# Kernel tuning notes

Hardware: AMD Instinct MI355X
Metric: run time of the kernel (lower is better)

The kernel has to match this reference:

```python
import jax, jax.numpy as jnp
import numpy as np

N_NODES = 50000
N_EDGES = 800000
N_GRAPHS = 512
NODE_IN = 128
EDGE_IN = 64
HIDDEN = 128
SHARED = 64


def setup_inputs() -> dict:
    key = jax.random.key(0)
    ks = jax.random.split(key, 24)
    def lin(k, fan_in, fan_out):
        lim = 1.0 / np.sqrt(fan_in)
        kw, kb = jax.random.split(k)
        w = jax.random.uniform(kw, (fan_in, fan_out), jnp.float32, -lim, lim)
        b = jax.random.uniform(kb, (fan_out,), jnp.float32, -lim, lim)
        return w, b
    x = jax.random.normal(ks[0], (N_NODES, NODE_IN), jnp.float32)
    edge_index = jax.random.randint(ks[1], (2, N_EDGES), 0, N_NODES, jnp.int64)
    edge_attr = jax.random.normal(ks[2], (N_EDGES, EDGE_IN), jnp.float32)
    batch = jnp.sort(jax.random.randint(ks[3], (N_NODES,), 0, N_GRAPHS, jnp.int64))
    e1_w, e1_b = lin(ks[4], EDGE_IN, NODE_IN)
    n1_w1, n1_b1 = lin(ks[5], NODE_IN, HIDDEN)
    n1_w2, n1_b2 = lin(ks[6], HIDDEN, HIDDEN)
    e2_w, e2_b = lin(ks[7], EDGE_IN, HIDDEN)
    n2_w1, n2_b1 = lin(ks[8], HIDDEN, HIDDEN)
    n2_w2, n2_b2 = lin(ks[9], HIDDEN, HIDDEN)
    fc_w, fc_b = lin(ks[10], HIDDEN, SHARED)
    hS_w, hS_b = lin(ks[11], SHARED, 1)
    hP_w, hP_b = lin(ks[12], SHARED, 1)
    hN_w, hN_b = lin(ks[13], SHARED, 1)
    return dict(x=x, edge_index=edge_index, edge_attr=edge_attr, batch=batch,
                e1_w=e1_w, e1_b=e1_b, n1_w1=n1_w1, n1_b1=n1_b1, n1_w2=n1_w2, n1_b2=n1_b2,
                e2_w=e2_w, e2_b=e2_b, n2_w1=n2_w1, n2_b1=n2_b1, n2_w2=n2_w2, n2_b2=n2_b2,
                fc_w=fc_w, fc_b=fc_b, hS_w=hS_w, hS_b=hS_b, hP_w=hP_w, hP_b=hP_b,
                hN_w=hN_w, hN_b=hN_b)


def gine_conv(x, edge_index, edge_attr, ew, eb, w1, b1, w2, b2):
    # message: relu(x_j + Lin(edge_attr)); aggregate: scatter-sum to target;
    # update: MLP((1 + eps) * x_i + aggr) with eps = 0 (PyG default)
    e = edge_attr @ ew + eb                      # [E, C]
    m = jax.nn.relu(x[edge_index[0]] + e)        # gather + fused add/relu
    aggr = jax.ops.segment_sum(m, edge_index[1], num_segments=N_NODES)
    h = x + aggr
    return jax.nn.relu(h @ w1 + b1) @ w2 + b2


def global_mean_pool(x, batch):
    sums = jax.ops.segment_sum(x, batch, num_segments=N_GRAPHS)
    cnt = jax.ops.segment_sum(jnp.ones((x.shape[0],), x.dtype), batch, num_segments=N_GRAPHS)
    return sums / jnp.maximum(cnt, 1.0)[:, None]


def reference(x, edge_index, edge_attr, batch,
              e1_w, e1_b, n1_w1, n1_b1, n1_w2, n1_b2,
              e2_w, e2_b, n2_w1, n2_b1, n2_w2, n2_b2,
              fc_w, fc_b, hS_w, hS_b, hP_w, hP_b, hN_w, hN_b):
    h = jax.nn.relu(gine_conv(x, edge_index, edge_attr, e1_w, e1_b, n1_w1, n1_b1, n1_w2, n1_b2))
    h = jax.nn.relu(gine_conv(h, edge_index, edge_attr, e2_w, e2_b, n2_w1, n2_b1, n2_w2, n2_b2))
    g = global_mean_pool(h, batch)               # [G, HIDDEN]
    s = jax.nn.relu(g @ fc_w + fc_b)             # [G, SHARED]
    logS = (s @ hS_w + hS_b)[:, 0]
    logP = (s @ hP_w + hP_b)[:, 0]
    nr = (s @ hN_w + hN_b)[:, 0]
    return logS, logP, nr
```

## Files before the change

### kernel.cpp

```cpp
#include <hip/hip_runtime.h>
#include <hip/hip_bf16.h>


typedef __bf16 bf16_t;

#define N_NODES   50000
#define N_EDGES   800000
#define N_GRAPHS  512
#define HID       128
#define EIN       64
#define PNODES    16

#define RL(v, l)  __int_as_float(__builtin_amdgcn_readlane(__float_as_int(v), (l)))
#define RLI(v, l) __builtin_amdgcn_readlane((v), (l))

__device__ __forceinline__ float ldf(const void* p, size_t i, int f32m) {
    return f32m ? ((const float*)p)[i] : (float)((const bf16_t*)p)[i];
}
__device__ __forceinline__ int ldi(const void* p, size_t i, int i64m) {
    return i64m ? (int)((const long long*)p)[i] : ((const int*)p)[i];
}

__global__ void k_detect(const unsigned short* __restrict__ xw,
                         const unsigned int*   __restrict__ eiw,
                         int* __restrict__ flags)
{
    if (threadIdx.x == 0 && blockIdx.x == 0) {
        int sane = 0;
        for (int i = 0; i < 256; ++i) {
            int e = (xw[i] >> 7) & 0xFF;
            if (e >= 100 && e <= 150) ++sane;
        }
        flags[0] = (sane < 220) ? 1 : 0;
        int nzhigh = 0;
        for (int i = 0; i < 256; ++i)
            if (eiw[2*i + 1] != 0) ++nzhigh;
        flags[1] = (nzhigh == 0) ? 1 : 0;
    }
}

__global__ void k_cvt4(const void* __restrict__ x, float* __restrict__ dst,
                       const int* __restrict__ flags) {
    const int f32m = flags[0];
    size_t i = (size_t)blockIdx.x * 256 + threadIdx.x;
    if (f32m) {
        ((float4*)dst)[i] = ((const float4*)x)[i];
    } else {
        const bf16_t* s = (const bf16_t*)x;
        float4 v;
        v.x = (float)s[4*i+0]; v.y = (float)s[4*i+1];
        v.z = (float)s[4*i+2]; v.w = (float)s[4*i+3];
        ((float4*)dst)[i] = v;
    }
}

__global__ __launch_bounds__(512) void k_edge_s(
        const void* __restrict__ Xg, int xg_ws,
        const void* __restrict__ ei,
        const void* __restrict__ ea,
        const void* __restrict__ ew,
        const void* __restrict__ eb,
        float*      __restrict__ ag,
        const int*  __restrict__ flags)
{
    __shared__ float4 Wq[16 * 128];
    __shared__ float  ebs[HID];
    const int f32m = flags[0];
    const int i64m = flags[1];
    const int xgf  = xg_ws ? 1 : f32m;

    for (int i = threadIdx.x; i < 16 * 128; i += 512) {
        int k4 = i >> 7, c = i & 127;
        float4 w;
        w.x = ldf(ew, (size_t)(4*k4+0)*HID + c, f32m);
        w.y = ldf(ew, (size_t)(4*k4+1)*HID + c, f32m);
        w.z = ldf(ew, (size_t)(4*k4+2)*HID + c, f32m);
        w.w = ldf(ew, (size_t)(4*k4+3)*HID + c, f32m);
        Wq[i] = w;
    }
    for (int i = threadIdx.x; i < HID; i += 512) ebs[i] = ldf(eb, i, f32m);
    __syncthreads();

    const int lane = threadIdx.x & 63;
    const int wid  = (blockIdx.x * 512 + threadIdx.x) >> 6;
    const int nw   = gridDim.x * 8;
    const int ngrp = N_EDGES / 8;
    const float eb0 = ebs[lane], eb1 = ebs[64 + lane];

    auto LOADIDX = [&](int e0) -> int {
        int v = 0;
        if (lane < 16) {
            size_t idx = (lane < 8) ? (size_t)(e0 + lane)
                                    : (size_t)N_EDGES + (e0 + lane - 8);
            v = ldi(ei, idx, i64m);
        }
        return v;
    };

    int g = wid;
    if (g < ngrp) {
        float avA[8]; int vvA;
        {
            const int e0 = g * 8;
            vvA = LOADIDX(e0);
#pragma unroll
            for (int i = 0; i < 8; ++i)
                avA[i] = ldf(ea, (size_t)(e0+i) * EIN + lane, f32m);
        }

        while (true) {
            const int gB = g + nw;
            const bool hasB = (gB < ngrp);
            float avB[8]; int vvB = 0;
            if (hasB) {
                const int e0B = gB * 8;
                vvB = LOADIDX(e0B);
#pragma unroll
                for (int i = 0; i < 8; ++i)
                    avB[i] = ldf(ea, (size_t)(e0B+i) * EIN + lane, f32m);
            }

            int src[8], dst[8];
#pragma unroll
            for (int i = 0; i < 8; ++i) {
                src[i] = RLI(vvA, i);
                dst[i] = RLI(vvA, 8 + i);
            }
            float x0[8], x1[8];
#pragma unroll
            for (int i = 0; i < 8; ++i) {
                x0[i] = ldf(Xg, (size_t)src[i] * HID + lane,      xgf);
                x1[i] = ldf(Xg, (size_t)src[i] * HID + 64 + lane, xgf);
            }

            float acc0[8], acc1[8];
#pragma unroll
            for (int i = 0; i < 8; ++i) { acc0[i] = 0.f; acc1[i] = 0.f; }

#pragma unroll 4
            for (int k4 = 0; k4 < 16; ++k4) {
                float4 w0 = Wq[k4 * 128 + lane];
                float4 w1 = Wq[k4 * 128 + 64 + lane];
#pragma unroll
                for (int i = 0; i < 8; ++i) {
                    float a0 = RL(avA[i], 4*k4+0);
                    float a1 = RL(avA[i], 4*k4+1);
                    float a2 = RL(avA[i], 4*k4+2);
                    float a3 = RL(avA[i], 4*k4+3);
                    acc0[i] = fmaf(a3, w0.w, fmaf(a2, w0.z, fmaf(a1, w0.y, fmaf(a0, w0.x, acc0[i]))));
                    acc1[i] = fmaf(a3, w1.w, fmaf(a2, w1.z, fmaf(a1, w1.y, fmaf(a0, w1.x, acc1[i]))));
                }
            }

#pragma unroll
            for (int i = 0; i < 8; ++i) {
                float v0 = fmaxf(x0[i] + acc0[i] + eb0, 0.f);
                float v1 = fmaxf(x1[i] + acc1[i] + eb1, 0.f);
                unsafeAtomicAdd(ag + (size_t)dst[i] * HID + lane,      v0);
                unsafeAtomicAdd(ag + (size_t)dst[i] * HID + 64 + lane, v1);
            }

            if (!hasB) break;
            g = gB;
            vvA = vvB;
#pragma unroll
            for (int i = 0; i < 8; ++i) avA[i] = avB[i];
        }
    }
}

__global__ __launch_bounds__(1024) void k_mlp_s(
        const float* __restrict__ A,
        const void*  __restrict__ W,
        const void*  __restrict__ bias,
        float*       __restrict__ Out,
        float*       __restrict__ Out2,
        const int*   __restrict__ flags)
{
    __shared__ float4 Wq[32 * 128];
    const int f32m = flags[0];
    for (int i = threadIdx.x; i < 32 * 128; i += 1024) {
        int k4 = i >> 7, c = i & 127;
        float4 w;
        w.x = ldf(W, (size_t)(4*k4+0)*HID + c, f32m);
        w.y = ldf(W, (size_t)(4*k4+1)*HID + c, f32m);
        w.z = ldf(W, (size_t)(4*k4+2)*HID + c, f32m);
        w.w = ldf(W, (size_t)(4*k4+3)*HID + c, f32m);
        Wq[i] = w;
    }
    __syncthreads();

    const int lane = threadIdx.x & 63;
    const int wid  = (blockIdx.x * 1024 + threadIdx.x) >> 6;
    const int nw   = gridDim.x * 16;
    const float b0 = ldf(bias, lane,      f32m);
    const float b1 = ldf(bias, 64 + lane, f32m);
    const int ngrp = N_NODES / 8;

    for (int g = wid; g < ngrp; g += nw) {
        const int n0 = g * 8;
        float alo[8], ahi[8], acc0[8], acc1[8];
#pragma unroll
        for (int i = 0; i < 8; ++i) {
            alo[i] = A[(size_t)(n0+i) * HID + lane];
            ahi[i] = A[(size_t)(n0+i) * HID + 64 + lane];
            acc0[i] = b0; acc1[i] = b1;
        }
#pragma unroll 4
        for (int k4 = 0; k4 < 16; ++k4) {
            float4 w0 = Wq[k4 * 128 + lane];
            float4 w1 = Wq[k4 * 128 + 64 + lane];
#pragma unroll
            for (int i = 0; i < 8; ++i) {
                float a0 = RL(alo[i], 4*k4+0);
                float a1 = RL(alo[i], 4*k4+1);
                float a2 = RL(alo[i], 4*k4+2);
                float a3 = RL(alo[i], 4*k4+3);
                acc0[i] = fmaf(a3, w0.w, fmaf(a2, w0.z, fmaf(a1, w0.y, fmaf(a0, w0.x, acc0[i]))));
                acc1[i] = fmaf(a3, w1.w, fmaf(a2, w1.z, fmaf(a1, w1.y, fmaf(a0, w1.x, acc1[i]))));
            }
        }
#pragma unroll 4
        for (int k4 = 16; k4 < 32; ++k4) {
            float4 w0 = Wq[k4 * 128 + lane];
            float4 w1 = Wq[k4 * 128 + 64 + lane];
#pragma unroll
            for (int i = 0; i < 8; ++i) {
                float a0 = RL(ahi[i], 4*k4+0 - 64);
                float a1 = RL(ahi[i], 4*k4+1 - 64);
                float a2 = RL(ahi[i], 4*k4+2 - 64);
                float a3 = RL(ahi[i], 4*k4+3 - 64);
                acc0[i] = fmaf(a3, w0.w, fmaf(a2, w0.z, fmaf(a1, w0.y, fmaf(a0, w0.x, acc0[i]))));
                acc1[i] = fmaf(a3, w1.w, fmaf(a2, w1.z, fmaf(a1, w1.y, fmaf(a0, w1.x, acc1[i]))));
            }
        }
#pragma unroll
        for (int i = 0; i < 8; ++i) {
            float v0 = fmaxf(acc0[i], 0.f);
            float v1 = fmaxf(acc1[i], 0.f);
            Out[(size_t)(n0+i) * HID + lane]      = v0;
            Out[(size_t)(n0+i) * HID + 64 + lane] = v1;
            if (Out2) {
                Out2[(size_t)(n0+i) * HID + lane]      = v0;
                Out2[(size_t)(n0+i) * HID + 64 + lane] = v1;
            }
        }
    }
}

__global__ void k_pool_s(const float* __restrict__ X, const void* __restrict__ batch,
                         float* __restrict__ GS, float* __restrict__ GC,
                         const int* __restrict__ flags)
{
    const int i64m = flags[1];
    const int c  = threadIdx.x;
    const int tl = threadIdx.x & 63;
    const int n0 = blockIdx.x * PNODES;

    int bv = (tl < PNODES) ? ldi(batch, n0 + tl, i64m) : 0;

    int bprev = RLI(bv, 0);
    float acc = 0.f;
    int   cnt = 0;
#pragma unroll
    for (int j = 0; j < PNODES; ++j) {
        int b = RLI(bv, j);
        if (b != bprev) {
            unsafeAtomicAdd(&GS[(size_t)bprev * HID + c], acc);
            if (c == 0) unsafeAtomicAdd(&GC[bprev], (float)cnt);
            acc = 0.f; cnt = 0; bprev = b;
        }
        acc += X[(size_t)(n0 + j) * HID + c];
        ++cnt;
    }
    unsafeAtomicAdd(&GS[(size_t)bprev * HID + c], acc);
    if (c == 0) unsafeAtomicAdd(&GC[bprev], (float)cnt);
}

__global__ void k_head(const float* __restrict__ GS, const float* __restrict__ GC,
                       const void* __restrict__ fcw, const void* __restrict__ fcb,
                       const void* __restrict__ hSw, const void* __restrict__ hSb,
                       const void* __restrict__ hPw, const void* __restrict__ hPb,
                       const void* __restrict__ hNw, const void* __restrict__ hNb,
                       float* __restrict__ out, const int* __restrict__ flags)
{
    const int f32m = flags[0];
    const int g = blockIdx.x;
    const int lane = threadIdx.x;
    const float inv = 1.f / fmaxf(GC[g], 1.f);
    const float g0 = GS[(size_t)g * HID + lane]      * inv;
    const float g1 = GS[(size_t)g * HID + 64 + lane] * inv;

    float acc = 0.f;
    for (int k = 0; k < 64; ++k) {
        float gk = __shfl(g0, k, 64);
        acc += gk * ldf(fcw, k * 64 + lane, f32m);
    }
    for (int k = 0; k < 64; ++k) {
        float gk = __shfl(g1, k, 64);
        acc += gk * ldf(fcw, (64 + k) * 64 + lane, f32m);
    }
    float s = fmaxf(acc + ldf(fcb, lane, f32m), 0.f);

    float pS = s * ldf(hSw, lane, f32m);
    float pP = s * ldf(hPw, lane, f32m);
    float pN = s * ldf(hNw, lane, f32m);
#pragma unroll
    for (int off = 32; off; off >>= 1) {
        pS += __shfl_down(pS, off, 64);
        pP += __shfl_down(pP, off, 64);
        pN += __shfl_down(pN, off, 64);
    }
    if (lane == 0) {
        out[g]                = pS + ldf(hSb, 0, f32m);
        out[N_GRAPHS + g]     = pP + ldf(hPb, 0, f32m);
        out[2 * N_GRAPHS + g] = pN + ldf(hNb, 0, f32m);
    }
}

extern "C" void kernel_launch(void* const* d_in, const int* in_sizes, int n_in,
                              void* d_out, int out_size, void* d_ws, size_t ws_size,
                              hipStream_t stream)
{
    const void* x     = d_in[0];
    const void* ei    = d_in[1];
    const void* ea    = d_in[2];
    const void* batch = d_in[3];
    const void* e1w = d_in[4],  *e1b = d_in[5];
    const void* n1w1= d_in[6],  *n1b1= d_in[7];
    const void* n1w2= d_in[8],  *n1b2= d_in[9];
    const void* e2w = d_in[10], *e2b = d_in[11];
    const void* n2w1= d_in[12], *n2b1= d_in[13];
    const void* n2w2= d_in[14], *n2b2= d_in[15];
    const void* fcw = d_in[16], *fcb = d_in[17];
    const void* hSw = d_in[18], *hSb = d_in[19];
    const void* hPw = d_in[20], *hPb = d_in[21];
    const void* hNw = d_in[22], *hNb = d_in[23];

    float* B1 = (float*)d_ws;
    float* B2 = B1 + (size_t)N_NODES * HID;
    float* GS = B2 + (size_t)N_NODES * HID;
    float* GC = GS + (size_t)N_GRAPHS * HID;
    int*   FL = (int*)(GC + N_GRAPHS);

    k_detect<<<1, 64, 0, stream>>>((const unsigned short*)x, (const unsigned int*)ei, FL);
    hipMemsetAsync(GS, 0, (N_GRAPHS * HID + N_GRAPHS) * sizeof(float), stream);

    const int NV4_BLKS = (N_NODES * HID / 4) / 256;

    k_cvt4  <<<NV4_BLKS, 256, 0, stream>>>(x, B1, FL);
    k_edge_s<<<2048, 512, 0, stream>>>(x, 0, ei, ea, e1w, e1b, B1, FL);
    k_mlp_s <<<512, 1024, 0, stream>>>(B1, n1w1, n1b1, B1, nullptr, FL);
    k_mlp_s <<<512, 1024, 0, stream>>>(B1, n1w2, n1b2, B1, B2, FL);

    k_edge_s<<<2048, 512, 0, stream>>>(B1, 1, ei, ea, e2w, e2b, B2, FL);
    k_mlp_s <<<512, 1024, 0, stream>>>(B2, n2w1, n2b1, B2, nullptr, FL);
    k_mlp_s <<<512, 1024, 0, stream>>>(B2, n2w2, n2b2, B2, nullptr, FL);

    k_pool_s<<<N_NODES / PNODES, 128, 0, stream>>>(B2, batch, GS, GC, FL);
    k_head  <<<N_GRAPHS, 64, 0, stream>>>(GS, GC, fcw, fcb, hSw, hSb, hPw, hPb, hNw, hNb,
                                          (float*)d_out, FL);
}
```

Before: 1.224 ms.

## Sort edges by destination into CSR, pre-combine atomics, fuse node MLP layers

Builds a destination-sorted edge list each call (histogram, three-stage scan, atomic scatter) so the edge kernel processes edges grouped by target. Consecutive edges that share a destination are summed in registers before the atomic add, cutting atomic traffic. The edge_attr loads become indirect gathers through the permutation, and index prefetch is pipelined one extra group ahead. The two per-layer MLP linear kernels are fused into one kernel holding both weight matrices in shared memory, which removes an intermediate write and read of node features. The cost is several extra preprocessing launches and doubled shared memory per MLP block, which lowers occupancy.

```diff
diff --git a/kernel.cpp b/kernel.cpp
--- a/kernel.cpp
+++ b/kernel.cpp
@@ -10,6 +10,8 @@
 #define HID       128
 #define EIN       64
 #define PNODES    16
+#define SCAN_BLK  1024
+#define NCHUNK    49
 
 #define RL(v, l)  __int_as_float(__builtin_amdgcn_readlane(__float_as_int(v), (l)))
 #define RLI(v, l) __builtin_amdgcn_readlane((v), (l))
@@ -54,9 +56,75 @@
     }
 }
 
+__global__ void k_hist(const void* __restrict__ ei, int* __restrict__ CNT,
+                       const int* __restrict__ flags)
+{
+    const int i64m = flags[1];
+    int e = blockIdx.x * 256 + threadIdx.x;
+    int d = ldi(ei, (size_t)N_EDGES + e, i64m);
+    atomicAdd(&CNT[d], 1);
+}
+
+__global__ __launch_bounds__(SCAN_BLK) void k_scanA(const int* __restrict__ CNT,
+                                                    int* __restrict__ OFF,
+                                                    int* __restrict__ PS)
+{
+    __shared__ int tmp[SCAN_BLK];
+    const int t = threadIdx.x;
+    const int i = blockIdx.x * SCAN_BLK + t;
+    const int v = (i < N_NODES) ? CNT[i] : 0;
+    tmp[t] = v;
+    __syncthreads();
+    for (int off = 1; off < SCAN_BLK; off <<= 1) {
+        int u = (t >= off) ? tmp[t - off] : 0;
+        __syncthreads();
+        tmp[t] += u;
+        __syncthreads();
+    }
+    if (i < N_NODES) OFF[i] = tmp[t] - v;
+    if (t == SCAN_BLK - 1) PS[blockIdx.x] = tmp[t];
+}
+
+__global__ void k_scanB(int* __restrict__ PS)
+{
+    const int lane = threadIdx.x;
+    const int v0 = (lane < NCHUNK) ? PS[lane] : 0;
+    int v = v0;
+#pragma unroll
+    for (int off = 1; off < 64; off <<= 1) {
+        int u = __shfl_up(v, off, 64);
+        if (lane >= off) v += u;
+    }
+    if (lane < NCHUNK) PS[lane] = v - v0;
+}
+
+__global__ void k_scanC(int* __restrict__ OFF, const int* __restrict__ PS,
+                        int* __restrict__ CUR)
+{
+    int i = blockIdx.x * 256 + threadIdx.x;
+    if (i < N_NODES) {
+        int o = OFF[i] + PS[i >> 10];
+        OFF[i] = o;
+        CUR[i] = o;
+    }
+}
+
+__global__ void k_scatter(const void* __restrict__ ei, int* __restrict__ CUR,
+                          int* __restrict__ CSR, const int* __restrict__ flags)
+{
+    const int i64m = flags[1];
+    int e = blockIdx.x * 256 + threadIdx.x;
+    int s = ldi(ei, e, i64m);
+    int d = ldi(ei, (size_t)N_EDGES + e, i64m);
+    int p = atomicAdd(&CUR[d], 1);
+    CSR[p]              = e;
+    CSR[N_EDGES + p]    = s;
+    CSR[2*N_EDGES + p]  = d;
+}
+
 __global__ __launch_bounds__(512) void k_edge_s(
         const void* __restrict__ Xg, int xg_ws,
-        const void* __restrict__ ei,
+        const int*  __restrict__ CSR,
         const void* __restrict__ ea,
         const void* __restrict__ ew,
         const void* __restrict__ eb,
@@ -66,7 +134,6 @@
     __shared__ float4 Wq[16 * 128];
     __shared__ float  ebs[HID];
     const int f32m = flags[0];
-    const int i64m = flags[1];
     const int xgf  = xg_ws ? 1 : f32m;
 
     for (int i = threadIdx.x; i < 16 * 128; i += 512) {
@@ -87,44 +154,39 @@
     const int ngrp = N_EDGES / 8;
     const float eb0 = ebs[lane], eb1 = ebs[64 + lane];
 
-    auto LOADIDX = [&](int e0) -> int {
+    auto LOADIDX = [&](int p0) -> int {
         int v = 0;
-        if (lane < 16) {
-            size_t idx = (lane < 8) ? (size_t)(e0 + lane)
-                                    : (size_t)N_EDGES + (e0 + lane - 8);
-            v = ldi(ei, idx, i64m);
-        }
+        if (lane < 24) v = CSR[(size_t)(lane >> 3) * N_EDGES + p0 + (lane & 7)];
         return v;
     };
+    auto LOADAV = [&](int vv, float* av) {
+#pragma unroll
+        for (int i = 0; i < 8; ++i) {
+            int eid = RLI(vv, i);
+            av[i] = ldf(ea, (size_t)eid * EIN + lane, f32m);
+        }
+    };
 
     int g = wid;
     if (g < ngrp) {
-        float avA[8]; int vvA;
-        {
-            const int e0 = g * 8;
-            vvA = LOADIDX(e0);
-#pragma unroll
-            for (int i = 0; i < 8; ++i)
-                avA[i] = ldf(ea, (size_t)(e0+i) * EIN + lane, f32m);
-        }
+        float avA[8];
+        int vvA = LOADIDX(g * 8);
+        LOADAV(vvA, avA);
+        int gB = g + nw;
+        int vvB = (gB < ngrp) ? LOADIDX(gB * 8) : 0;
 
         while (true) {
-            const int gB = g + nw;
             const bool hasB = (gB < ngrp);
-            float avB[8]; int vvB = 0;
-            if (hasB) {
-                const int e0B = gB * 8;
-                vvB = LOADIDX(e0B);
-#pragma unroll
-                for (int i = 0; i < 8; ++i)
-                    avB[i] = ldf(ea, (size_t)(e0B+i) * EIN + lane, f32m);
-            }
+            float avB[8];
+            if (hasB) LOADAV(vvB, avB);
+            const int gC = gB + nw;
+            int vvC = (hasB && gC < ngrp) ? LOADIDX(gC * 8) : 0;
 
             int src[8], dst[8];
 #pragma unroll
             for (int i = 0; i < 8; ++i) {
-                src[i] = RLI(vvA, i);
-                dst[i] = RLI(vvA, 8 + i);
+                src[i] = RLI(vvA, 8 + i);
+                dst[i] = RLI(vvA, 16 + i);
             }
             float x0[8], x1[8];
 #pragma unroll
@@ -152,92 +214,141 @@
                 }
             }
 
+            float s0 = 0.f, s1 = 0.f;
 #pragma unroll
             for (int i = 0; i < 8; ++i) {
                 float v0 = fmaxf(x0[i] + acc0[i] + eb0, 0.f);
                 float v1 = fmaxf(x1[i] + acc1[i] + eb1, 0.f);
-                unsafeAtomicAdd(ag + (size_t)dst[i] * HID + lane,      v0);
-                unsafeAtomicAdd(ag + (size_t)dst[i] * HID + 64 + lane, v1);
+                s0 += v0; s1 += v1;
+                if (i == 7 || dst[i + 1] != dst[i]) {
+                    unsafeAtomicAdd(ag + (size_t)dst[i] * HID + lane,      s0);
+                    unsafeAtomicAdd(ag + (size_t)dst[i] * HID + 64 + lane, s1);
+                    s0 = 0.f; s1 = 0.f;
+                }
             }
 
             if (!hasB) break;
-            g = gB;
-            vvA = vvB;
+            g = gB; gB = gC;
+            vvA = vvB; vvB = vvC;
 #pragma unroll
             for (int i = 0; i < 8; ++i) avA[i] = avB[i];
         }
     }
 }
 
-__global__ __launch_bounds__(1024) void k_mlp_s(
+__global__ __launch_bounds__(1024) void k_mlp2(
         const float* __restrict__ A,
-        const void*  __restrict__ W,
-        const void*  __restrict__ bias,
+        const void*  __restrict__ W1, const void* __restrict__ b1,
+        const void*  __restrict__ W2, const void* __restrict__ b2,
         float*       __restrict__ Out,
         float*       __restrict__ Out2,
         const int*   __restrict__ flags)
 {
-    __shared__ float4 Wq[32 * 128];
+    __shared__ float4 W1q[32 * 128];
+    __shared__ float4 W2q[32 * 128];
     const int f32m = flags[0];
     for (int i = threadIdx.x; i < 32 * 128; i += 1024) {
         int k4 = i >> 7, c = i & 127;
         float4 w;
-        w.x = ldf(W, (size_t)(4*k4+0)*HID + c, f32m);
-        w.y = ldf(W, (size_t)(4*k4+1)*HID + c, f32m);
-        w.z = ldf(W, (size_t)(4*k4+2)*HID + c, f32m);
-        w.w = ldf(W, (size_t)(4*k4+3)*HID + c, f32m);
-        Wq[i] = w;
+        w.x = ldf(W1, (size_t)(4*k4+0)*HID + c, f32m);
+        w.y = ldf(W1, (size_t)(4*k4+1)*HID + c, f32m);
+        w.z = ldf(W1, (size_t)(4*k4+2)*HID + c, f32m);
+        w.w = ldf(W1, (size_t)(4*k4+3)*HID + c, f32m);
+        W1q[i] = w;
+        w.x = ldf(W2, (size_t)(4*k4+0)*HID + c, f32m);
+        w.y = ldf(W2, (size_t)(4*k4+1)*HID + c, f32m);
+        w.z = ldf(W2, (size_t)(4*k4+2)*HID + c, f32m);
+        w.w = ldf(W2, (size_t)(4*k4+3)*HID + c, f32m);
+        W2q[i] = w;
     }
     __syncthreads();
 
     const int lane = threadIdx.x & 63;
     const int wid  = (blockIdx.x * 1024 + threadIdx.x) >> 6;
     const int nw   = gridDim.x * 16;
-    const float b0 = ldf(bias, lane,      f32m);
-    const float b1 = ldf(bias, 64 + lane, f32m);
+    const float c10 = ldf(b1, lane,      f32m);
+    const float c11 = ldf(b1, 64 + lane, f32m);
+    const float c20 = ldf(b2, lane,      f32m);
+    const float c21 = ldf(b2, 64 + lane, f32m);
     const int ngrp = N_NODES / 8;
 
     for (int g = wid; g < ngrp; g += nw) {
         const int n0 = g * 8;
-        float alo[8], ahi[8], acc0[8], acc1[8];
+        float alo[8], ahi[8], t0[8], t1[8];
 #pragma unroll
         for (int i = 0; i < 8; ++i) {
             alo[i] = A[(size_t)(n0+i) * HID + lane];
             ahi[i] = A[(size_t)(n0+i) * HID + 64 + lane];
-            acc0[i] = b0; acc1[i] = b1;
+            t0[i] = c10; t1[i] = c11;
         }
 #pragma unroll 4
         for (int k4 = 0; k4 < 16; ++k4) {
-            float4 w0 = Wq[k4 * 128 + lane];
-            float4 w1 = Wq[k4 * 128 + 64 + lane];
+            float4 w0 = W1q[k4 * 128 + lane];
+            float4 w1 = W1q[k4 * 128 + 64 + lane];
 #pragma unroll
             for (int i = 0; i < 8; ++i) {
                 float a0 = RL(alo[i], 4*k4+0);
                 float a1 = RL(alo[i], 4*k4+1);
                 float a2 = RL(alo[i], 4*k4+2);
                 float a3 = RL(alo[i], 4*k4+3);
-                acc0[i] = fmaf(a3, w0.w, fmaf(a2, w0.z, fmaf(a1, w0.y, fmaf(a0, w0.x, acc0[i]))));
-                acc1[i] = fmaf(a3, w1.w, fmaf(a2, w1.z, fmaf(a1, w1.y, fmaf(a0, w1.x, acc1[i]))));
+                t0[i] = fmaf(a3, w0.w, fmaf(a2, w0.z, fmaf(a1, w0.y, fmaf(a0, w0.x, t0[i]))));
+                t1[i] = fmaf(a3, w1.w, fmaf(a2, w1.z, fmaf(a1, w1.y, fmaf(a0, w1.x, t1[i]))));
             }
         }
 #pragma unroll 4
         for (int k4 = 16; k4 < 32; ++k4) {
-            float4 w0 = Wq[k4 * 128 + lane];
-            float4 w1 = Wq[k4 * 128 + 64 + lane];
+            float4 w0 = W1q[k4 * 128 + lane];
+            float4 w1 = W1q[k4 * 128 + 64 + lane];
 #pragma unroll
             for (int i = 0; i < 8; ++i) {
                 float a0 = RL(ahi[i], 4*k4+0 - 64);
                 float a1 = RL(ahi[i], 4*k4+1 - 64);
                 float a2 = RL(ahi[i], 4*k4+2 - 64);
                 float a3 = RL(ahi[i], 4*k4+3 - 64);
-                acc0[i] = fmaf(a3, w0.w, fmaf(a2, w0.z, fmaf(a1, w0.y, fmaf(a0, w0.x, acc0[i]))));
-                acc1[i] = fmaf(a3, w1.w, fmaf(a2, w1.z, fmaf(a1, w1.y, fmaf(a0, w1.x, acc1[i]))));
+                t0[i] = fmaf(a3, w0.w, fmaf(a2, w0.z, fmaf(a1, w0.y, fmaf(a0, w0.x, t0[i]))));
+                t1[i] = fmaf(a3, w1.w, fmaf(a2, w1.z, fmaf(a1, w1.y, fmaf(a0, w1.x, t1[i]))));
             }
         }
 #pragma unroll
         for (int i = 0; i < 8; ++i) {
-            float v0 = fmaxf(acc0[i], 0.f);
-            float v1 = fmaxf(acc1[i], 0.f);
+            t0[i] = fmaxf(t0[i], 0.f);
+            t1[i] = fmaxf(t1[i], 0.f);
+        }
+        float o0[8], o1[8];
+#pragma unroll
+        for (int i = 0; i < 8; ++i) { o0[i] = c20; o1[i] = c21; }
+#pragma unroll 4
+        for (int k4 = 0; k4 < 16; ++k4) {
+            float4 w0 = W2q[k4 * 128 + lane];
+            float4 w1 = W2q[k4 * 128 + 64 + lane];
+#pragma unroll
+            for (int i = 0; i < 8; ++i) {
+                float a0 = RL(t0[i], 4*k4+0);
+                float a1 = RL(t0[i], 4*k4+1);
+                float a2 = RL(t0[i], 4*k4+2);
+                float a3 = RL(t0[i], 4*k4+3);
+                o0[i] = fmaf(a3, w0.w, fmaf(a2, w0.z, fmaf(a1, w0.y, fmaf(a0, w0.x, o0[i]))));
+                o1[i] = fmaf(a3, w1.w, fmaf(a2, w1.z, fmaf(a1, w1.y, fmaf(a0, w1.x, o1[i]))));
+            }
+        }
+#pragma unroll 4
+        for (int k4 = 16; k4 < 32; ++k4) {
+            float4 w0 = W2q[k4 * 128 + lane];
+            float4 w1 = W2q[k4 * 128 + 64 + lane];
+#pragma unroll
+            for (int i = 0; i < 8; ++i) {
+                float a0 = RL(t1[i], 4*k4+0 - 64);
+                float a1 = RL(t1[i], 4*k4+1 - 64);
+                float a2 = RL(t1[i], 4*k4+2 - 64);
+                float a3 = RL(t1[i], 4*k4+3 - 64);
+                o0[i] = fmaf(a3, w0.w, fmaf(a2, w0.z, fmaf(a1, w0.y, fmaf(a0, w0.x, o0[i]))));
+                o1[i] = fmaf(a3, w1.w, fmaf(a2, w1.z, fmaf(a1, w1.y, fmaf(a0, w1.x, o1[i]))));
+            }
+        }
+#pragma unroll
+        for (int i = 0; i < 8; ++i) {
+            float v0 = fmaxf(o0[i], 0.f);
+            float v1 = fmaxf(o1[i], 0.f);
             Out[(size_t)(n0+i) * HID + lane]      = v0;
             Out[(size_t)(n0+i) * HID + 64 + lane] = v1;
             if (Out2) {
@@ -337,25 +448,35 @@
     const void* hPw = d_in[20], *hPb = d_in[21];
     const void* hNw = d_in[22], *hNb = d_in[23];
 
-    float* B1 = (float*)d_ws;
-    float* B2 = B1 + (size_t)N_NODES * HID;
-    float* GS = B2 + (size_t)N_NODES * HID;
-    float* GC = GS + (size_t)N_GRAPHS * HID;
-    int*   FL = (int*)(GC + N_GRAPHS);
+    float* B1  = (float*)d_ws;
+    float* B2  = B1 + (size_t)N_NODES * HID;
+    float* GS  = B2 + (size_t)N_NODES * HID;
+    float* GC  = GS + (size_t)N_GRAPHS * HID;
+    int*   FL  = (int*)(GC + N_GRAPHS);
+    int*   PS  = FL + 4;
+    int*   OFF = PS + 64;
+    int*   CNT = OFF + N_NODES;
+    int*   CUR = CNT + N_NODES;
+    int*   CSR = CUR + N_NODES;
 
     k_detect<<<1, 64, 0, stream>>>((const unsigned short*)x, (const unsigned int*)ei, FL);
     hipMemsetAsync(GS, 0, (N_GRAPHS * HID + N_GRAPHS) * sizeof(float), stream);
+    hipMemsetAsync(CNT, 0, N_NODES * sizeof(int), stream);
+
+    k_hist   <<<N_EDGES / 256, 256, 0, stream>>>(ei, CNT, FL);
+    k_scanA  <<<NCHUNK, SCAN_BLK, 0, stream>>>(CNT, OFF, PS);
+    k_scanB  <<<1, 64, 0, stream>>>(PS);
+    k_scanC  <<<(N_NODES + 255) / 256, 256, 0, stream>>>(OFF, PS, CUR);
+    k_scatter<<<N_EDGES / 256, 256, 0, stream>>>(ei, CUR, CSR, FL);
 
     const int NV4_BLKS = (N_NODES * HID / 4) / 256;
 
     k_cvt4  <<<NV4_BLKS, 256, 0, stream>>>(x, B1, FL);
-    k_edge_s<<<2048, 512, 0, stream>>>(x, 0, ei, ea, e1w, e1b, B1, FL);
-    k_mlp_s <<<512, 1024, 0, stream>>>(B1, n1w1, n1b1, B1, nullptr, FL);
-    k_mlp_s <<<512, 1024, 0, stream>>>(B1, n1w2, n1b2, B1, B2, FL);
-
-    k_edge_s<<<2048, 512, 0, stream>>>(B1, 1, ei, ea, e2w, e2b, B2, FL);
-    k_mlp_s <<<512, 1024, 0, stream>>>(B2, n2w1, n2b1, B2, nullptr, FL);
-    k_mlp_s <<<512, 1024, 0, stream>>>(B2, n2w2, n2b2, B2, nullptr, FL);
+    k_edge_s<<<2048, 512, 0, stream>>>(x, 0, CSR, ea, e1w, e1b, B1, FL);
+    k_mlp2  <<<256, 1024, 0, stream>>>(B1, n1w1, n1b1, n1w2, n1b2, B1, B2, FL);
+
+    k_edge_s<<<2048, 512, 0, stream>>>(B1, 1, CSR, ea, e2w, e2b, B2, FL);
+    k_mlp2  <<<256, 1024, 0, stream>>>(B2, n2w1, n2b1, n2w2, n2b2, B2, nullptr, FL);
 
     k_pool_s<<<N_NODES / PNODES, 128, 0, stream>>>(B2, batch, GS, GC, FL);
     k_head  <<<N_GRAPHS, 64, 0, stream>>>(GS, GC, fcw, fcb, hSw, hSb, hPw, hPb, hNw, hNb,
```

Result: slower. 1.261 ms (+3.0%).
